# Kernel optimization log

Hardware: AMD Instinct MI355X
Metric: run time of the kernel (lower is better)

## Reference

```python
import jax, jax.numpy as jnp
import numpy as np

T, B, D_MODEL = 2048, 4, 1024
EXPAND, D_STATE, D_CONV = 2, 16, 4
D_INNER = EXPAND * D_MODEL
DT_RANK = -(-D_MODEL // 16)  # ceil(d_model/16) = 64


def setup_inputs() -> dict:
    key = jax.random.key(0)
    ks = jax.random.split(key, 10)
    g = lambda k, shape, scale: jax.random.normal(k, shape, jnp.float32) * scale
    return {
        "x": g(ks[0], (T, B, D_MODEL), 1.0),
        "W_in": g(ks[1], (D_MODEL, 2 * D_INNER), 0.02),          # in_proj (no bias)
        "conv_w": g(ks[2], (D_INNER, D_CONV), 0.2),              # depthwise conv weight
        "conv_b": g(ks[3], (D_INNER,), 0.1),                     # depthwise conv bias
        "W_x": g(ks[4], (D_INNER, DT_RANK + 2 * D_STATE), 0.02), # x_proj (no bias)
        "W_dt": g(ks[5], (DT_RANK, D_INNER), 0.05),              # dt_proj weight
        "b_dt": g(ks[6], (D_INNER,), 0.1),                       # dt_proj bias
        "A_log": jnp.log(jnp.tile(jnp.arange(1, D_STATE + 1, dtype=jnp.float32), (D_INNER, 1))),
        "D": jnp.ones((D_INNER,), jnp.float32),
        "W_out": g(ks[9], (D_INNER, D_MODEL), 0.02),             # out_proj (no bias)
    }


def reference(x, W_in, conv_w, conv_b, W_x, W_dt, b_dt, A_log, D, W_out):
    # x: (t, b, c) -> (b, t, c)
    xb = jnp.transpose(x, (1, 0, 2))
    # input projection -> (b, t, 2*d_inner), split into ssm branch u and gate res
    u, res = jnp.split(xb @ W_in, 2, axis=-1)
    # causal depthwise conv over time (torch Conv1d groups=d_inner, left pad d_conv-1)
    uc = jnp.transpose(u, (0, 2, 1))                        # (b, d_inner, t)
    uc = jax.lax.conv_general_dilated(
        uc, conv_w[:, None, :], (1,), [(D_CONV - 1, 0)],
        feature_group_count=D_INNER)
    u = jax.nn.silu(jnp.transpose(uc, (0, 2, 1)) + conv_b)  # (b, t, d_inner)
    # selective SSM parameters
    A = -jnp.exp(A_log)                                     # (d_inner, d_state)
    x_dbl = u @ W_x                                         # (b, t, dt_rank + 2n)
    delta, Bm, Cm = jnp.split(x_dbl, [DT_RANK, DT_RANK + D_STATE], axis=-1)
    delta = jax.nn.softplus(delta @ W_dt + b_dt)            # (b, t, d_inner)
    # selective scan over time; state h: (b, d_inner, d_state)
    def step(h, inp):
        d_t, B_t, C_t, u_t = inp                            # (b,d),(b,n),(b,n),(b,d)
        dA = jnp.exp(d_t[..., None] * A)                    # (b, d, n)
        h = dA * h + (d_t * u_t)[..., None] * B_t[:, None, :]
        y = jnp.einsum('bdn,bn->bd', h, C_t)
        return h, y
    h0 = jnp.zeros((B, D_INNER, D_STATE), x.dtype)
    seq = (jnp.transpose(delta, (1, 0, 2)), jnp.transpose(Bm, (1, 0, 2)),
           jnp.transpose(Cm, (1, 0, 2)), jnp.transpose(u, (1, 0, 2)))
    _, ys = jax.lax.scan(step, h0, seq)                     # (t, b, d_inner)
    y = jnp.transpose(ys, (1, 0, 2)) + u * D                # skip connection
    y = y * jax.nn.silu(res)                                # gate
    out = y @ W_out                                         # (b, t, c)
    return jnp.transpose(out, (1, 0, 2))                    # (t, b, c)
```

## Files before the change

kernel.cpp:

```cpp
#include <hip/hip_runtime.h>
#include <hip/hip_bf16.h>
#include <stdint.h>

#define T_LEN   2048
#define BATCH   4
#define DMODEL  1024
#define DINNER  2048
#define DSTATE  16
#define DTRANK  64
#define MROWS   (BATCH*T_LEN)
#define NCHUNK  16
#define CLEN    (T_LEN / NCHUNK)
#define PF      8

typedef __bf16 bf16x8_t __attribute__((ext_vector_type(8)));
typedef float  f32x4_t  __attribute__((ext_vector_type(4)));

__device__ __forceinline__ uint16_t f2b(float f) {
    uint32_t u = __float_as_uint(f);
    u += 0x7fffu + ((u >> 16) & 1u);
    return (uint16_t)(u >> 16);
}
__device__ __forceinline__ float b2f(uint16_t h) {
    return __uint_as_float(((uint32_t)h) << 16);
}

__device__ __forceinline__ void gload16(const void* g, void* l) {
    __builtin_amdgcn_global_load_lds(
        (const __attribute__((address_space(1))) void*)g,
        (__attribute__((address_space(3))) void*)l, 16, 0, 0);
}

__global__ __launch_bounds__(256) void convert_x_kernel(
    const float* __restrict__ x, uint16_t* __restrict__ xb)
{
    int tb = blockIdx.x;
    int t = tb >> 2, b = tb & 3;
    int c = threadIdx.x * 4;
    const float4 v = *(const float4*)(x + ((size_t)tb) * DMODEL + c);
    uint16_t* dst = xb + ((size_t)(b * T_LEN + t)) * DMODEL + c;
    uint2 p;
    p.x = (uint32_t)f2b(v.x) | ((uint32_t)f2b(v.y) << 16);
    p.y = (uint32_t)f2b(v.z) | ((uint32_t)f2b(v.w) << 16);
    *(uint2*)dst = p;
}

__global__ __launch_bounds__(256) void transpose_cvt_kernel(
    const float* __restrict__ src, uint16_t* __restrict__ dst,
    int R, int C, int Cpad)
{
    __shared__ float tile[32][33];
    int r0 = blockIdx.x * 32;
    int c0 = blockIdx.y * 32;
    int tx = threadIdx.x, ty = threadIdx.y;
#pragma unroll
    for (int i = 0; i < 32; i += 8) {
        int r = r0 + ty + i, c = c0 + tx;
        tile[ty + i][tx] = (r < R && c < C) ? src[(size_t)r * C + c] : 0.f;
    }
    __syncthreads();
#pragma unroll
    for (int i = 0; i < 32; i += 8) {
        int dr = c0 + ty + i;
        int dc = r0 + tx;
        if (dr < Cpad && dc < R) dst[(size_t)dr * R + dc] = f2b(tile[tx][ty + i]);
    }
}

#define EPI_BF16  0
#define EPI_F32G  1
#define EPI_SP    2
#define EPI_REMAP 3

template <int EPI, bool SPLITK>
__global__ __launch_bounds__(256) void gemm_bt_kernel(
    const uint16_t* __restrict__ A, const uint16_t* __restrict__ Bt,
    void* __restrict__ CoutBase, const float* __restrict__ bias,
    int N, int K, int ldc, int ksplit)
{
    __shared__ uint16_t As[128 * 32];
    __shared__ uint16_t Bs[128 * 32];

    int tid = threadIdx.x;
    int bm = blockIdx.x * 128, bn = blockIdx.y * 128;
    int kbeg = SPLITK ? blockIdx.z * ksplit : 0;
    int kend = SPLITK ? kbeg + ksplit : K;
    void* Cout = SPLITK
        ? (void*)((float*)CoutBase + (size_t)blockIdx.z * MROWS * ldc)
        : CoutBase;

    const uint16_t* ap0 = A  + (size_t)(bm + (tid >> 2)) * K + kbeg + (tid & 3) * 8;
    const uint16_t* ap1 = ap0 + (size_t)64 * K;
    const uint16_t* bp0 = Bt + (size_t)(bn + (tid >> 2)) * K + kbeg + (tid & 3) * 8;
    const uint16_t* bp1 = bp0 + (size_t)64 * K;

    f32x4_t acc[4][4];
#pragma unroll
    for (int i = 0; i < 4; i++)
#pragma unroll
        for (int j = 0; j < 4; j++) acc[i][j] = (f32x4_t){0.f, 0.f, 0.f, 0.f};

    int wid = tid >> 6, lane = tid & 63;
    int wm = (wid & 1) * 64, wn = (wid >> 1) * 64;
    int lr = lane & 15, lq = lane >> 4;
    const uint16_t* Afrag = &As[(wm + lr) * 32 + lq * 8];
    const uint16_t* Bfrag = &Bs[(wn + lr) * 32 + lq * 8];

    for (int k0 = kbeg; k0 < kend; k0 += 32) {
        __syncthreads();
        gload16(ap0, &As[(size_t)tid * 8]);
        gload16(ap1, &As[(size_t)(tid + 256) * 8]);
        gload16(bp0, &Bs[(size_t)tid * 8]);
        gload16(bp1, &Bs[(size_t)(tid + 256) * 8]);
        ap0 += 32; ap1 += 32; bp0 += 32; bp1 += 32;
        __syncthreads();

        bf16x8_t av[4], bv[4];
#pragma unroll
        for (int i = 0; i < 4; i++) av[i] = *(const bf16x8_t*)(Afrag + i * 512);
#pragma unroll
        for (int j = 0; j < 4; j++) bv[j] = *(const bf16x8_t*)(Bfrag + j * 512);
#pragma unroll
        for (int i = 0; i < 4; i++)
#pragma unroll
            for (int j = 0; j < 4; j++)
                acc[i][j] = __builtin_amdgcn_mfma_f32_16x16x32_bf16(
                    av[i], bv[j], acc[i][j], 0, 0, 0);
    }

#pragma unroll
    for (int i = 0; i < 4; i++) {
#pragma unroll
        for (int j = 0; j < 4; j++) {
            int col = bn + wn + j * 16 + lr;
#pragma unroll
            for (int r = 0; r < 4; r++) {
                int row = bm + wm + i * 16 + lq * 4 + r;
                float v = acc[i][j][r];
                if (EPI == EPI_BF16) {
                    ((uint16_t*)Cout)[(size_t)row * ldc + col] = f2b(v);
                } else if (EPI == EPI_F32G) {
                    if (col < N) ((float*)Cout)[(size_t)row * ldc + col] = v;
                } else if (EPI == EPI_SP) {
                    float xv = v + bias[col];
                    float sp = (xv > 15.f) ? xv : __logf(1.f + __expf(xv));
                    ((uint16_t*)Cout)[(size_t)row * ldc + col] = f2b(sp);
                } else {
                    int bb = row >> 11, tt = row & (T_LEN - 1);
                    ((float*)Cout)[((size_t)(tt * BATCH + bb)) * ldc + col] = v;
                }
            }
        }
    }
}

#define CROWS 16

__global__ __launch_bounds__(256) void conv_silu_kernel(
    const uint16_t* __restrict__ z, const float* __restrict__ cw,
    const float* __restrict__ cb, uint16_t* __restrict__ u)
{
    int c0 = threadIdx.x * 8;
    int m0 = blockIdx.x * CROWS;

    float w[8][4], bias[8];
#pragma unroll
    for (int c = 0; c < 8; ++c)
        *(float4*)w[c] = *(const float4*)(cw + (size_t)(c0 + c) * 4);
    *(float4*)&bias[0] = *(const float4*)(cb + c0);
    *(float4*)&bias[4] = *(const float4*)(cb + c0 + 4);

    float fw[4][8];
    bool seqstart = (m0 & (T_LEN - 1)) == 0;
#pragma unroll
    for (int j = 0; j < 3; ++j) {
        int m = m0 - 3 + j;
        if (seqstart) {
#pragma unroll
            for (int c = 0; c < 8; ++c) fw[j + 1][c] = 0.f;
        } else {
            uint4 v = *(const uint4*)(z + (size_t)m * 4096 + c0);
            fw[j + 1][0] = b2f((uint16_t)(v.x & 0xffff)); fw[j + 1][1] = b2f((uint16_t)(v.x >> 16));
            fw[j + 1][2] = b2f((uint16_t)(v.y & 0xffff)); fw[j + 1][3] = b2f((uint16_t)(v.y >> 16));
            fw[j + 1][4] = b2f((uint16_t)(v.z & 0xffff)); fw[j + 1][5] = b2f((uint16_t)(v.z >> 16));
            fw[j + 1][6] = b2f((uint16_t)(v.w & 0xffff)); fw[j + 1][7] = b2f((uint16_t)(v.w >> 16));
        }
    }

#pragma unroll
    for (int t = 0; t < CROWS; ++t) {
        int m = m0 + t;
        int s = t & 3;
        uint4 v = *(const uint4*)(z + (size_t)m * 4096 + c0);
        fw[s][0] = b2f((uint16_t)(v.x & 0xffff)); fw[s][1] = b2f((uint16_t)(v.x >> 16));
        fw[s][2] = b2f((uint16_t)(v.y & 0xffff)); fw[s][3] = b2f((uint16_t)(v.y >> 16));
        fw[s][4] = b2f((uint16_t)(v.z & 0xffff)); fw[s][5] = b2f((uint16_t)(v.z >> 16));
        fw[s][6] = b2f((uint16_t)(v.w & 0xffff)); fw[s][7] = b2f((uint16_t)(v.w >> 16));
        uint16_t out[8];
#pragma unroll
        for (int c = 0; c < 8; ++c) {
            float a = bias[c];
#pragma unroll
            for (int j = 0; j < 4; ++j)
                a = fmaf(fw[(t + 1 + j) & 3][c], w[c][j], a);
            float sv = a / (1.f + __expf(-a));
            out[c] = f2b(sv);
        }
        uint4 o;
        o.x = (uint32_t)out[0] | ((uint32_t)out[1] << 16);
        o.y = (uint32_t)out[2] | ((uint32_t)out[3] << 16);
        o.z = (uint32_t)out[4] | ((uint32_t)out[5] << 16);
        o.w = (uint32_t)out[6] | ((uint32_t)out[7] << 16);
        *(uint4*)(u + (size_t)m * DINNER + c0) = o;
    }
}

__global__ __launch_bounds__(128) void reduce_xdbl_kernel(
    const float* __restrict__ xpart, float* __restrict__ xdbl,
    uint16_t* __restrict__ dr16)
{
    int m = blockIdx.x, r = threadIdx.x;
    if (r >= 96) return;
    const size_t stride = (size_t)MROWS * 96;
    size_t idx = (size_t)m * 96 + r;
    float s = xpart[idx] + xpart[stride + idx]
            + xpart[2 * stride + idx] + xpart[3 * stride + idx];
    xdbl[idx] = s;
    if (r < DTRANK) dr16[(size_t)m * DTRANK + r] = f2b(s);
}

#define LOG2E 1.44269504088896340736f

__global__ __launch_bounds__(256) void scan_part1_kernel(
    const uint16_t* __restrict__ delta16, const uint16_t* __restrict__ u16,
    const float* __restrict__ xdbl, const float* __restrict__ A_log,
    float* __restrict__ Pws, float* __restrict__ Qws)
{
    __shared__ float lds_b[CLEN][16];
    int tid = threadIdx.x;
    int d = blockIdx.x * 256 + tid;
    int b = blockIdx.y, c = blockIdx.z;
    size_t mbase = (size_t)b * T_LEN + (size_t)c * CLEN;

    {
        int r = tid >> 1, pair = tid & 1;
        const float4* src = (const float4*)(xdbl + (mbase + r) * 96 + 64 + pair * 8);
        float4* dst = (float4*)&lds_b[r][pair * 8];
        dst[0] = src[0]; dst[1] = src[1];
    }

    float ae[DSTATE];
#pragma unroll
    for (int n = 0; n < DSTATE; ++n)
        ae[n] = -__expf(A_log[d * DSTATE + n]) * LOG2E;
    bool fastexp = true;
#pragma unroll
    for (int n = 1; n < DSTATE; ++n)
        fastexp = fastexp && (fabsf(ae[n] - (n + 1) * ae[0]) <= 1e-4f * fabsf(ae[n]));

    float h[DSTATE];
#pragma unroll
    for (int n = 0; n < DSTATE; ++n) h[n] = 0.f;
    float sdelta = 0.f;

    uint16_t dpf[PF], upf[PF];
#pragma unroll
    for (int t = 0; t < PF; ++t) {
        size_t m = mbase + t;
        dpf[t] = delta16[m * DINNER + d];
        upf[t] = u16[m * DINNER + d];
    }
    __syncthreads();

    if (fastexp) {
#pragma unroll 8
        for (int t = 0; t < CLEN; ++t) {
            int slot = t & (PF - 1);
            float delta = b2f(dpf[slot]);
            float du    = delta * b2f(upf[slot]);
            int tn = t + PF; tn = tn < CLEN ? tn : CLEN - 1;
            size_t mn = mbase + tn;
            dpf[slot] = delta16[mn * DINNER + d];
            upf[slot] = u16[mn * DINNER + d];
            float Bv[DSTATE];
            *(float4*)&Bv[0]  = *(const float4*)&lds_b[t][0];
            *(float4*)&Bv[4]  = *(const float4*)&lds_b[t][4];
            *(float4*)&Bv[8]  = *(const float4*)&lds_b[t][8];
            *(float4*)&Bv[12] = *(const float4*)&lds_b[t][12];
            float q = __builtin_amdgcn_exp2f(delta * ae[0]);
            float w = 1.f;
            sdelta += delta;
#pragma unroll
            for (int n = 0; n < DSTATE; ++n) {
                w *= q;
                h[n] = fmaf(w, h[n], du * Bv[n]);
            }
        }
    } else {
#pragma unroll 8
        for (int t = 0; t < CLEN; ++t) {
            int slot = t & (PF - 1);
            float delta = b2f(dpf[slot]);
            float du    = delta * b2f(upf[slot]);
            int tn = t + PF; tn = tn < CLEN ? tn : CLEN - 1;
            size_t mn = mbase + tn;
            dpf[slot] = delta16[mn * DINNER + d];
            upf[slot] = u16[mn * DINNER + d];
            float Bv[DSTATE];
            *(float4*)&Bv[0]  = *(const float4*)&lds_b[t][0];
            *(float4*)&Bv[4]  = *(const float4*)&lds_b[t][4];
            *(float4*)&Bv[8]  = *(const float4*)&lds_b[t][8];
            *(float4*)&Bv[12] = *(const float4*)&lds_b[t][12];
            sdelta += delta;
#pragma unroll
            for (int n = 0; n < DSTATE; ++n) {
                float w = __builtin_amdgcn_exp2f(delta * ae[n]);
                h[n] = fmaf(w, h[n], du * Bv[n]);
            }
        }
    }

    float P[DSTATE];
#pragma unroll
    for (int n = 0; n < DSTATE; ++n)
        P[n] = __builtin_amdgcn_exp2f(ae[n] * sdelta);
    float* Pp = Pws + (((size_t)c * BATCH + b) * DINNER + d) * DSTATE;
    float* Qp = Qws + (((size_t)c * BATCH + b) * DINNER + d) * DSTATE;
#pragma unroll
    for (int n = 0; n < DSTATE; n += 4) {
        *(float4*)(Pp + n) = *(float4*)&P[n];
        *(float4*)(Qp + n) = *(float4*)&h[n];
    }
}

__global__ __launch_bounds__(256) void scan_combine_kernel(
    float* __restrict__ Pws, const float* __restrict__ Qws)
{
    size_t i = (size_t)blockIdx.x * 256 + threadIdx.x;
    const size_t stride = (size_t)BATCH * DINNER * DSTATE;
    float h = 0.f;
#pragma unroll
    for (int c = 0; c < NCHUNK; ++c) {
        float P = Pws[c * stride + i];
        float Q = Qws[c * stride + i];
        Pws[c * stride + i] = h;
        h = fmaf(P, h, Q);
    }
}

__global__ __launch_bounds__(256) void scan_part3_kernel(
    const uint16_t* __restrict__ delta16, const uint16_t* __restrict__ u16,
    const float* __restrict__ xdbl, const uint16_t* __restrict__ z16,
    const float* __restrict__ A_log, const float* __restrict__ Dvec,
    const float* __restrict__ H0ws, uint16_t* __restrict__ y16)
{
    __shared__ float lds_bc[CLEN][32];
    int tid = threadIdx.x;
    int d = blockIdx.x * 256 + tid;
    int b = blockIdx.y, c = blockIdx.z;
    size_t mbase = (size_t)b * T_LEN + (size_t)c * CLEN;

    {
        int r = tid >> 1, half = tid & 1;
        const float4* src = (const float4*)(xdbl + (mbase + r) * 96 + 64 + half * 16);
        float4* dst = (float4*)&lds_bc[r][half * 16];
        dst[0] = src[0]; dst[1] = src[1]; dst[2] = src[2]; dst[3] = src[3];
    }

    float ae[DSTATE];
#pragma unroll
    for (int n = 0; n < DSTATE; ++n)
        ae[n] = -__expf(A_log[d * DSTATE + n]) * LOG2E;
    bool fastexp = true;
#pragma unroll
    for (int n = 1; n < DSTATE; ++n)
        fastexp = fastexp && (fabsf(ae[n] - (n + 1) * ae[0]) <= 1e-4f * fabsf(ae[n]));
    float Dd = Dvec[d];

    float h[DSTATE];
    size_t hbase = (((size_t)c * BATCH + b) * DINNER + d) * DSTATE;
#pragma unroll
    for (int n = 0; n < DSTATE; n += 4)
        *(float4*)&h[n] = *(const float4*)(H0ws + hbase + n);

    uint16_t dpf[PF], upf[PF], rpf[PF];
#pragma unroll
    for (int t = 0; t < PF; ++t) {
        size_t m = mbase + t;
        dpf[t] = delta16[m * DINNER + d];
        upf[t] = u16[m * DINNER + d];
        rpf[t] = z16[m * 4096 + DINNER + d];
    }
    __syncthreads();

    if (fastexp) {
#pragma unroll 8
        for (int t = 0; t < CLEN; ++t) {
            int slot = t & (PF - 1);
            float delta = b2f(dpf[slot]);
            float uu    = b2f(upf[slot]);
            float rg    = b2f(rpf[slot]);
            int tn = t + PF; tn = tn < CLEN ? tn : CLEN - 1;
            size_t mn = mbase + tn;
            dpf[slot] = delta16[mn * DINNER + d];
            upf[slot] = u16[mn * DINNER + d];
            rpf[slot] = z16[mn * 4096 + DINNER + d];
            float du = delta * uu;
            float Bv[DSTATE], Cv[DSTATE];
            *(float4*)&Bv[0]  = *(const float4*)&lds_bc[t][0];
            *(float4*)&Bv[4]  = *(const float4*)&lds_bc[t][4];
            *(float4*)&Bv[8]  = *(const float4*)&lds_bc[t][8];
            *(float4*)&Bv[12] = *(const float4*)&lds_bc[t][12];
            *(float4*)&Cv[0]  = *(const float4*)&lds_bc[t][16];
            *(float4*)&Cv[4]  = *(const float4*)&lds_bc[t][20];
            *(float4*)&Cv[8]  = *(const float4*)&lds_bc[t][24];
            *(float4*)&Cv[12] = *(const float4*)&lds_bc[t][28];
            float q = __builtin_amdgcn_exp2f(delta * ae[0]);
            float w = 1.f, y = 0.f;
#pragma unroll
            for (int n = 0; n < DSTATE; ++n) {
                w *= q;
                h[n] = fmaf(w, h[n], du * Bv[n]);
                y = fmaf(h[n], Cv[n], y);
            }
            y = fmaf(uu, Dd, y);
            float sig = 1.f / (1.f + __expf(-rg));
            y16[(mbase + t) * DINNER + d] = f2b(y * rg * sig);
        }
    } else {
#pragma unroll 8
        for (int t = 0; t < CLEN; ++t) {
            int slot = t & (PF - 1);
            float delta = b2f(dpf[slot]);
            float uu    = b2f(upf[slot]);
            float rg    = b2f(rpf[slot]);
            int tn = t + PF; tn = tn < CLEN ? tn : CLEN - 1;
            size_t mn = mbase + tn;
            dpf[slot] = delta16[mn * DINNER + d];
            upf[slot] = u16[mn * DINNER + d];
            rpf[slot] = z16[mn * 4096 + DINNER + d];
            float du = delta * uu;
            float Bv[DSTATE], Cv[DSTATE];
            *(float4*)&Bv[0]  = *(const float4*)&lds_bc[t][0];
            *(float4*)&Bv[4]  = *(const float4*)&lds_bc[t][4];
            *(float4*)&Bv[8]  = *(const float4*)&lds_bc[t][8];
            *(float4*)&Bv[12] = *(const float4*)&lds_bc[t][12];
            *(float4*)&Cv[0]  = *(const float4*)&lds_bc[t][16];
            *(float4*)&Cv[4]  = *(const float4*)&lds_bc[t][20];
            *(float4*)&Cv[8]  = *(const float4*)&lds_bc[t][24];
            *(float4*)&Cv[12] = *(const float4*)&lds_bc[t][28];
            float y = 0.f;
#pragma unroll
            for (int n = 0; n < DSTATE; ++n) {
                float w = __builtin_amdgcn_exp2f(delta * ae[n]);
                h[n] = fmaf(w, h[n], du * Bv[n]);
                y = fmaf(h[n], Cv[n], y);
            }
            y = fmaf(uu, Dd, y);
            float sig = 1.f / (1.f + __expf(-rg));
            y16[(mbase + t) * DINNER + d] = f2b(y * rg * sig);
        }
    }
}

extern "C" void kernel_launch(void* const* d_in, const int* in_sizes, int n_in,
                              void* d_out, int out_size, void* d_ws, size_t ws_size,
                              hipStream_t stream)
{
    const float* x     = (const float*)d_in[0];
    const float* W_in  = (const float*)d_in[1];
    const float* cw    = (const float*)d_in[2];
    const float* cb    = (const float*)d_in[3];
    const float* W_x   = (const float*)d_in[4];
    const float* W_dt  = (const float*)d_in[5];
    const float* b_dt  = (const float*)d_in[6];
    const float* A_log = (const float*)d_in[7];
    const float* Dv    = (const float*)d_in[8];
    const float* W_out = (const float*)d_in[9];

    char* ws = (char*)d_ws;
    size_t off = 0;
    uint16_t* xb16    = (uint16_t*)(ws + off); off += (size_t)MROWS * DMODEL * 2;
    uint16_t* WinT    = (uint16_t*)(ws + off); off += (size_t)4096 * 1024 * 2;
    uint16_t* WoutT   = (uint16_t*)(ws + off); off += (size_t)1024 * 2048 * 2;
    uint16_t* WxT     = (uint16_t*)(ws + off); off += (size_t)128 * 2048 * 2;
    uint16_t* WdtT    = (uint16_t*)(ws + off); off += (size_t)2048 * 64 * 2;
    uint16_t* z16     = (uint16_t*)(ws + off); off += (size_t)MROWS * 4096 * 2;
    uint16_t* u16     = (uint16_t*)(ws + off); off += (size_t)MROWS * DINNER * 2;
    float*    xdbl    = (float*)(ws + off);    off += (size_t)MROWS * 96 * 4;
    uint16_t* dr16    = (uint16_t*)(ws + off); off += (size_t)MROWS * 64 * 2;
    uint16_t* delta16 = (uint16_t*)(ws + off); off += (size_t)MROWS * DINNER * 2;
    uint16_t* y16     = (uint16_t*)(ws + off); off += (size_t)MROWS * DINNER * 2;

    float* xpart = (float*)xb16;
    float* Pws   = (float*)xb16;
    float* Qws   = Pws + (size_t)NCHUNK * BATCH * DINNER * DSTATE;

    dim3 tb(32, 8);
    convert_x_kernel<<<MROWS, 256, 0, stream>>>(x, xb16);
    transpose_cvt_kernel<<<dim3(32, 128), tb, 0, stream>>>(W_in,  WinT,  1024, 4096, 4096);
    transpose_cvt_kernel<<<dim3(64, 32),  tb, 0, stream>>>(W_out, WoutT, 2048, 1024, 1024);
    transpose_cvt_kernel<<<dim3(64, 4),   tb, 0, stream>>>(W_x,   WxT,   2048, 96, 128);
    transpose_cvt_kernel<<<dim3(2, 64),   tb, 0, stream>>>(W_dt,  WdtT,  64, 2048, 2048);

    gemm_bt_kernel<EPI_BF16, false><<<dim3(64, 32), 256, 0, stream>>>(
        xb16, WinT, z16, nullptr, 4096, 1024, 4096, 0);
    conv_silu_kernel<<<MROWS / CROWS, 256, 0, stream>>>(z16, cw, cb, u16);
    gemm_bt_kernel<EPI_F32G, true><<<dim3(64, 1, 4), 256, 0, stream>>>(
        u16, WxT, xpart, nullptr, 96, 2048, 96, 512);
    reduce_xdbl_kernel<<<MROWS, 128, 0, stream>>>(xpart, xdbl, dr16);
    gemm_bt_kernel<EPI_SP, false><<<dim3(64, 16), 256, 0, stream>>>(
        dr16, WdtT, delta16, b_dt, 2048, 64, 2048, 0);

    scan_part1_kernel<<<dim3(DINNER / 256, BATCH, NCHUNK), 256, 0, stream>>>(
        delta16, u16, xdbl, A_log, Pws, Qws);
    scan_combine_kernel<<<BATCH * DINNER * DSTATE / 256, 256, 0, stream>>>(
        Pws, Qws);
    scan_part3_kernel<<<dim3(DINNER / 256, BATCH, NCHUNK), 256, 0, stream>>>(
        delta16, u16, xdbl, z16, A_log, Dv, Pws, y16);

    gemm_bt_kernel<EPI_REMAP, false><<<dim3(64, 8), 256, 0, stream>>>(
        y16, WoutT, d_out, nullptr, 1024, 2048, 1024, 0);
}
```

Baseline: 420.2 us.

## Deepen GEMM K-tile with swizzled LDS, merge weight transposes, double scan chunks

The GEMM now stages 64-wide K slices instead of 32, with an XOR swizzle on the LDS column index to avoid bank conflicts. This halves the barrier and loop overhead per K and doubles LDS use per block. The four weight transpose launches are merged into one kernel to cut launch overhead. The scan uses 32 chunks instead of 16 for more parallelism, at the cost of a longer combine step. The P/Q workspace moves into the output buffer, and the LDS preload indexing is adjusted to the shorter chunk length.

```diff
diff --git a/kernel.cpp b/kernel.cpp
--- a/kernel.cpp
+++ b/kernel.cpp
@@ -9,7 +9,7 @@
 #define DSTATE  16
 #define DTRANK  64
 #define MROWS   (BATCH*T_LEN)
-#define NCHUNK  16
+#define NCHUNK  32
 #define CLEN    (T_LEN / NCHUNK)
 #define PF      8
 
@@ -45,14 +45,22 @@
     *(uint2*)dst = p;
 }
 
-__global__ __launch_bounds__(256) void transpose_cvt_kernel(
-    const float* __restrict__ src, uint16_t* __restrict__ dst,
-    int R, int C, int Cpad)
+__global__ __launch_bounds__(256) void transpose4_kernel(
+    const float* __restrict__ W_in,  const float* __restrict__ W_out,
+    const float* __restrict__ W_x,   const float* __restrict__ W_dt,
+    uint16_t* __restrict__ WinT, uint16_t* __restrict__ WoutT,
+    uint16_t* __restrict__ WxT,  uint16_t* __restrict__ WdtT)
 {
     __shared__ float tile[32][33];
-    int r0 = blockIdx.x * 32;
-    int c0 = blockIdx.y * 32;
-    int tx = threadIdx.x, ty = threadIdx.y;
+    int blk = blockIdx.x;
+    const float* src; uint16_t* dst; int R, C, Cpad, gx;
+    if (blk < 4096)      { src=W_in;  dst=WinT;  R=1024; C=4096; Cpad=4096; gx=32;  }
+    else if (blk < 6144) { src=W_out; dst=WoutT; R=2048; C=1024; Cpad=1024; gx=64;  blk -= 4096; }
+    else if (blk < 6400) { src=W_x;   dst=WxT;   R=2048; C=96;   Cpad=128;  gx=64;  blk -= 6144; }
+    else                 { src=W_dt;  dst=WdtT;  R=64;   C=2048; Cpad=2048; gx=2;   blk -= 6400; }
+    int r0 = (blk % gx) * 32;
+    int c0 = (blk / gx) * 32;
+    int tx = threadIdx.x & 31, ty = threadIdx.x >> 5;
 #pragma unroll
     for (int i = 0; i < 32; i += 8) {
         int r = r0 + ty + i, c = c0 + tx;
@@ -78,8 +86,8 @@
     void* __restrict__ CoutBase, const float* __restrict__ bias,
     int N, int K, int ldc, int ksplit)
 {
-    __shared__ uint16_t As[128 * 32];
-    __shared__ uint16_t Bs[128 * 32];
+    __shared__ uint16_t As[128 * 64];
+    __shared__ uint16_t Bs[128 * 64];
 
     int tid = threadIdx.x;
     int bm = blockIdx.x * 128, bn = blockIdx.y * 128;
@@ -89,10 +97,10 @@
         ? (void*)((float*)CoutBase + (size_t)blockIdx.z * MROWS * ldc)
         : CoutBase;
 
-    const uint16_t* ap0 = A  + (size_t)(bm + (tid >> 2)) * K + kbeg + (tid & 3) * 8;
-    const uint16_t* ap1 = ap0 + (size_t)64 * K;
-    const uint16_t* bp0 = Bt + (size_t)(bn + (tid >> 2)) * K + kbeg + (tid & 3) * 8;
-    const uint16_t* bp1 = bp0 + (size_t)64 * K;
+    int srow = tid >> 3;
+    int slc  = (tid & 7) ^ (srow & 7);
+    const uint16_t* ap = A  + (size_t)(bm + srow) * K + kbeg + slc * 8;
+    const uint16_t* bp = Bt + (size_t)(bn + srow) * K + kbeg + slc * 8;
 
     f32x4_t acc[4][4];
 #pragma unroll
@@ -103,23 +111,38 @@
     int wid = tid >> 6, lane = tid & 63;
     int wm = (wid & 1) * 64, wn = (wid >> 1) * 64;
     int lr = lane & 15, lq = lane >> 4;
-    const uint16_t* Afrag = &As[(wm + lr) * 32 + lq * 8];
-    const uint16_t* Bfrag = &Bs[(wn + lr) * 32 + lq * 8];
-
-    for (int k0 = kbeg; k0 < kend; k0 += 32) {
+    int pc0 = (lq ^ (lr & 7)) * 8;
+    int pc1 = ((lq ^ 4) ^ (lr & 7)) * 8;
+    const uint16_t* AfS0 = &As[(wm + lr) * 64 + pc0];
+    const uint16_t* AfS1 = &As[(wm + lr) * 64 + pc1];
+    const uint16_t* BfS0 = &Bs[(wn + lr) * 64 + pc0];
+    const uint16_t* BfS1 = &Bs[(wn + lr) * 64 + pc1];
+
+    for (int k0 = kbeg; k0 < kend; k0 += 64) {
         __syncthreads();
-        gload16(ap0, &As[(size_t)tid * 8]);
-        gload16(ap1, &As[(size_t)(tid + 256) * 8]);
-        gload16(bp0, &Bs[(size_t)tid * 8]);
-        gload16(bp1, &Bs[(size_t)(tid + 256) * 8]);
-        ap0 += 32; ap1 += 32; bp0 += 32; bp1 += 32;
+#pragma unroll
+        for (int p = 0; p < 4; p++) {
+            gload16(ap + (size_t)p * 32 * K, &As[(size_t)(p * 256 + tid) * 8]);
+            gload16(bp + (size_t)p * 32 * K, &Bs[(size_t)(p * 256 + tid) * 8]);
+        }
+        ap += 64; bp += 64;
         __syncthreads();
 
         bf16x8_t av[4], bv[4];
 #pragma unroll
-        for (int i = 0; i < 4; i++) av[i] = *(const bf16x8_t*)(Afrag + i * 512);
-#pragma unroll
-        for (int j = 0; j < 4; j++) bv[j] = *(const bf16x8_t*)(Bfrag + j * 512);
+        for (int i = 0; i < 4; i++) av[i] = *(const bf16x8_t*)(AfS0 + i * 1024);
+#pragma unroll
+        for (int j = 0; j < 4; j++) bv[j] = *(const bf16x8_t*)(BfS0 + j * 1024);
+#pragma unroll
+        for (int i = 0; i < 4; i++)
+#pragma unroll
+            for (int j = 0; j < 4; j++)
+                acc[i][j] = __builtin_amdgcn_mfma_f32_16x16x32_bf16(
+                    av[i], bv[j], acc[i][j], 0, 0, 0);
+#pragma unroll
+        for (int i = 0; i < 4; i++) av[i] = *(const bf16x8_t*)(AfS1 + i * 1024);
+#pragma unroll
+        for (int j = 0; j < 4; j++) bv[j] = *(const bf16x8_t*)(BfS1 + j * 1024);
 #pragma unroll
         for (int i = 0; i < 4; i++)
 #pragma unroll
@@ -243,10 +266,9 @@
     size_t mbase = (size_t)b * T_LEN + (size_t)c * CLEN;
 
     {
-        int r = tid >> 1, pair = tid & 1;
-        const float4* src = (const float4*)(xdbl + (mbase + r) * 96 + 64 + pair * 8);
-        float4* dst = (float4*)&lds_b[r][pair * 8];
-        dst[0] = src[0]; dst[1] = src[1];
+        int r = tid >> 2, q = tid & 3;
+        *(float4*)&lds_b[r][q * 4] =
+            *(const float4*)(xdbl + (mbase + r) * 96 + 64 + q * 4);
     }
 
     float ae[DSTATE];
@@ -361,10 +383,10 @@
     size_t mbase = (size_t)b * T_LEN + (size_t)c * CLEN;
 
     {
-        int r = tid >> 1, half = tid & 1;
-        const float4* src = (const float4*)(xdbl + (mbase + r) * 96 + 64 + half * 16);
-        float4* dst = (float4*)&lds_bc[r][half * 16];
-        dst[0] = src[0]; dst[1] = src[1]; dst[2] = src[2]; dst[3] = src[3];
+        int r = tid >> 2, q = tid & 3;
+        const float4* src = (const float4*)(xdbl + (mbase + r) * 96 + 64 + q * 8);
+        float4* dst = (float4*)&lds_bc[r][q * 8];
+        dst[0] = src[0]; dst[1] = src[1];
     }
 
     float ae[DSTATE];
@@ -493,15 +515,12 @@
     uint16_t* y16     = (uint16_t*)(ws + off); off += (size_t)MROWS * DINNER * 2;
 
     float* xpart = (float*)xb16;
-    float* Pws   = (float*)xb16;
+    float* Pws   = (float*)d_out;
     float* Qws   = Pws + (size_t)NCHUNK * BATCH * DINNER * DSTATE;
 
-    dim3 tb(32, 8);
     convert_x_kernel<<<MROWS, 256, 0, stream>>>(x, xb16);
-    transpose_cvt_kernel<<<dim3(32, 128), tb, 0, stream>>>(W_in,  WinT,  1024, 4096, 4096);
-    transpose_cvt_kernel<<<dim3(64, 32),  tb, 0, stream>>>(W_out, WoutT, 2048, 1024, 1024);
-    transpose_cvt_kernel<<<dim3(64, 4),   tb, 0, stream>>>(W_x,   WxT,   2048, 96, 128);
-    transpose_cvt_kernel<<<dim3(2, 64),   tb, 0, stream>>>(W_dt,  WdtT,  64, 2048, 2048);
+    transpose4_kernel<<<6528, 256, 0, stream>>>(
+        W_in, W_out, W_x, W_dt, WinT, WoutT, WxT, WdtT);
 
     gemm_bt_kernel<EPI_BF16, false><<<dim3(64, 32), 256, 0, stream>>>(
         xb16, WinT, z16, nullptr, 4096, 1024, 4096, 0);
```

Result: faster. 391.8 us (-6.8%).
